# Kernel optimization log

Measured on AMD Instinct MI355X. Metric: run time of the kernel, lower is better.

The kernel has to match this reference:

```python
import jax, jax.numpy as jnp
import numpy as np

B, S, D = 16, 2048, 128


def setup_inputs() -> dict:
    key = jax.random.key(0)
    kq, kk, kv = jax.random.split(key, 3)
    return {
        "queries": jax.random.normal(kq, (B, S, D), dtype=jnp.float32),
        "keys": jax.random.normal(kk, (B, S, D), dtype=jnp.float32),
        "values": jax.random.normal(kv, (B, S, D), dtype=jnp.float32),
        "mask": jnp.zeros((B, S, S), dtype=bool),  # True -> masked out
    }


def reference(queries, keys, values, mask):
    d_k = queries.shape[-1]
    scale = 1.0 / np.sqrt(d_k).astype(np.float32)
    # scores: [B, S, S]
    scores = jnp.einsum("bqd,bkd->bqk", queries, keys) * scale
    scores = jnp.where(mask, -jnp.inf, scores)
    attn_weights = jax.nn.softmax(scores, axis=-1)
    # dropout prob = 0.0 (eval), identity
    output = jnp.einsum("bqk,bkd->bqd", attn_weights, values)
    return output
```

## Files before the change

### kernel.cpp

```cpp
#include <hip/hip_runtime.h>
#include <hip/hip_bf16.h>

#define SEQ    2048
#define DIM    128
#define NBATCH 16
#define KVB    64
#define HALFS  (SEQ / 2)
#define NTILE  (HALFS / KVB)
#define QW     16
#define NWAVE  8
#define QB     (QW * NWAVE)
#define NROW   (NBATCH * SEQ)
#define TELEM  (KVB * DIM)

typedef __bf16 bf16x8 __attribute__((ext_vector_type(8)));
typedef float  f32x4  __attribute__((ext_vector_type(4)));
typedef unsigned int uint;

#define LOG2E  1.44269504088896340736f
#define NEGINF (-__builtin_inff())

#define CVT_PK(d, lo, hi) asm("v_cvt_pk_bf16_f32 %0, %1, %2" : "=v"(d) : "v"(lo), "v"(hi))
#define SWAP32(x, y) asm("v_permlane32_swap_b32 %0, %1" : "+v"(x), "+v"(y))
#define SWAP16(x, y) asm("v_permlane16_swap_b32 %0, %1" : "+v"(x), "+v"(y))

typedef const __attribute__((address_space(1))) uint* gup;
typedef       __attribute__((address_space(3))) uint* lup;
#define GLDS16(g, l) __builtin_amdgcn_global_load_lds((gup)(g), (lup)(l), 16, 0, 0)

__global__ __launch_bounds__(512)
void sdpa_prep(const float* __restrict__ Kg, const float* __restrict__ Vg,
               __bf16* __restrict__ Kb, __bf16* __restrict__ Vb)
{
    const int tile = (int)blockIdx.x;
    const int tid  = (int)threadIdx.x;
    const size_t row0 = (size_t)tile * KVB;

    {
        const int kr = tid >> 3;
        const int c2 = (tid & 7) * 2;
        const int kx = kr & 7;
        const float* src = Kg + (row0 + kr) * DIM;
        __bf16* dst = Kb + ((size_t)tile * KVB + kr) * DIM;
        #pragma unroll
        for (int c = 0; c < 2; ++c) {
            const int ci = c2 + c;
            const int sc = ci ^ kx;
            const float4 a = *(const float4*)(src + sc * 8);
            const float4 b = *(const float4*)(src + sc * 8 + 4);
            bf16x8 h;
            h[0]=(__bf16)a.x; h[1]=(__bf16)a.y; h[2]=(__bf16)a.z; h[3]=(__bf16)a.w;
            h[4]=(__bf16)b.x; h[5]=(__bf16)b.y; h[6]=(__bf16)b.z; h[7]=(__bf16)b.w;
            *(bf16x8*)(dst + ci * 8) = h;
        }
    }
    {
        const int vd  = tid & 127;
        const int vks = tid >> 7;
        const int vx  = vd & 7;
        const float* src = Vg + row0 * DIM + vd;
        __bf16* dst = Vb + (size_t)tile * TELEM + (size_t)vd * KVB;
        #pragma unroll
        for (int c = 0; c < 2; ++c) {
            const int ck = vks * 2 + c;
            const int ci = ck ^ vx;
            bf16x8 h;
            #pragma unroll
            for (int j = 0; j < 8; ++j) h[j] = (__bf16)src[(size_t)(ck * 8 + j) * DIM];
            *(bf16x8*)(dst + ci * 8) = h;
        }
    }
}

__global__ __launch_bounds__(512, 4)
void sdpa_main(const float* __restrict__ Qg, const __bf16* __restrict__ Kbf,
               const __bf16* __restrict__ Vbf, const unsigned char* __restrict__ Mg,
               float* __restrict__ Uw, float* __restrict__ Lw)
{
    __shared__ __bf16 Ksh[2][TELEM];
    __shared__ __bf16 Vsh[2][TELEM];

    const int tid  = (int)threadIdx.x;
    const int wid  = tid >> 6;
    const int lane = tid & 63;
    const int lg   = lane >> 4;
    const int lr   = lane & 15;

    const int bid  = (int)blockIdx.x;
    const int nbid = (bid & 7) * 64 + (bid >> 3);
    const int half = nbid & 1;
    const int qt   = nbid >> 1;
    const int bb   = qt >> 4;
    const int q0w  = (qt & 15) * QB + wid * QW;

    const float qscale = 0.08838834764831845f * LOG2E;

    bf16x8 aq[4];
    {
        const float* qrow = Qg + ((size_t)(bb * SEQ + q0w + lr)) * DIM;
        #pragma unroll
        for (int kb = 0; kb < 4; ++kb) {
            const float4 f0 = *(const float4*)(qrow + kb * 32 + lg * 8);
            const float4 f1 = *(const float4*)(qrow + kb * 32 + lg * 8 + 4);
            bf16x8 h;
            h[0] = (__bf16)(f0.x * qscale); h[1] = (__bf16)(f0.y * qscale);
            h[2] = (__bf16)(f0.z * qscale); h[3] = (__bf16)(f0.w * qscale);
            h[4] = (__bf16)(f1.x * qscale); h[5] = (__bf16)(f1.y * qscale);
            h[6] = (__bf16)(f1.z * qscale); h[7] = (__bf16)(f1.w * qscale);
            aq[kb] = h;
        }
    }

    const __bf16* Kt0 = Kbf + (size_t)(bb * 32 + half * 16) * TELEM;
    const __bf16* Vt0 = Vbf + (size_t)(bb * 32 + half * 16) * TELEM;
    const unsigned char* Mrow = Mg + (size_t)bb * SEQ * SEQ
                              + (size_t)(q0w + lr) * SEQ + half * HALFS;

    uint mn0, mn1, mn2, mn3;

    const int woff0 = wid * 1024;
    const int woff1 = 8192 + wid * 1024;
    const int loff  = lane * 16;

    auto issue = [&](int t, int b) {
        const char* Ks = (const char*)(Kt0 + (size_t)t * TELEM);
        const char* Vs = (const char*)(Vt0 + (size_t)t * TELEM);
        char* Kd = (char*)Ksh[b];
        char* Vd = (char*)Vsh[b];
        GLDS16(Ks + woff0 + loff, Kd + woff0);
        GLDS16(Ks + woff1 + loff, Kd + woff1);
        GLDS16(Vs + woff0 + loff, Vd + woff0);
        GLDS16(Vs + woff1 + loff, Vd + woff1);
        const unsigned char* ms = Mrow + t * KVB + lg * 4;
        mn0 = *(const uint*)(ms);
        mn1 = *(const uint*)(ms + 16);
        mn2 = *(const uint*)(ms + 32);
        mn3 = *(const uint*)(ms + 48);
    };

    issue(0, 0);

    f32x4 acc[8];
    #pragma unroll
    for (int i = 0; i < 8; ++i) acc[i] = (f32x4)(0.0f);
    float l_run = 0.0f;

    const int kxr = lr & 7;

    for (int t = 0; t < NTILE; ++t) {
        asm volatile("s_waitcnt vmcnt(0)" ::: "memory");
        __syncthreads();
        const uint mw0 = mn0, mw1 = mn1, mw2 = mn2, mw3 = mn3;
        if (t + 1 < NTILE) issue(t + 1, (t + 1) & 1);

        const bf16x8* const Kc = (const bf16x8*)Ksh[t & 1];
        const bf16x8* const Vc = (const bf16x8*)Vsh[t & 1];

        f32x4 s0 = (f32x4)(0.0f), s1 = (f32x4)(0.0f);
        f32x4 s2 = (f32x4)(0.0f), s3 = (f32x4)(0.0f);
        __builtin_amdgcn_s_setprio(1);
        #pragma unroll
        for (int kb = 0; kb < 4; ++kb) {
            const int ch = (kb * 4 + lg) ^ kxr;
            const bf16x8 a0 = Kc[(lr)      * 16 + ch];
            const bf16x8 a1 = Kc[(16 + lr) * 16 + ch];
            const bf16x8 a2 = Kc[(32 + lr) * 16 + ch];
            const bf16x8 a3 = Kc[(48 + lr) * 16 + ch];
            s0 = __builtin_amdgcn_mfma_f32_16x16x32_bf16(a0, aq[kb], s0, 0, 0, 0);
            s1 = __builtin_amdgcn_mfma_f32_16x16x32_bf16(a1, aq[kb], s1, 0, 0, 0);
            s2 = __builtin_amdgcn_mfma_f32_16x16x32_bf16(a2, aq[kb], s2, 0, 0, 0);
            s3 = __builtin_amdgcn_mfma_f32_16x16x32_bf16(a3, aq[kb], s3, 0, 0, 0);
        }
        __builtin_amdgcn_s_setprio(0);

        if (mw0) {
            if (mw0 & 0x000000ffu) s0[0] = NEGINF;
            if (mw0 & 0x0000ff00u) s0[1] = NEGINF;
            if (mw0 & 0x00ff0000u) s0[2] = NEGINF;
            if (mw0 & 0xff000000u) s0[3] = NEGINF;
        }
        if (mw1) {
            if (mw1 & 0x000000ffu) s1[0] = NEGINF;
            if (mw1 & 0x0000ff00u) s1[1] = NEGINF;
            if (mw1 & 0x00ff0000u) s1[2] = NEGINF;
            if (mw1 & 0xff000000u) s1[3] = NEGINF;
        }
        if (mw2) {
            if (mw2 & 0x000000ffu) s2[0] = NEGINF;
            if (mw2 & 0x0000ff00u) s2[1] = NEGINF;
            if (mw2 & 0x00ff0000u) s2[2] = NEGINF;
            if (mw2 & 0xff000000u) s2[3] = NEGINF;
        }
        if (mw3) {
            if (mw3 & 0x000000ffu) s3[0] = NEGINF;
            if (mw3 & 0x0000ff00u) s3[1] = NEGINF;
            if (mw3 & 0x00ff0000u) s3[2] = NEGINF;
            if (mw3 & 0xff000000u) s3[3] = NEGINF;
        }

        float ps = 0.0f;
        #pragma unroll
        for (int r = 0; r < 4; ++r) { s0[r] = __builtin_amdgcn_exp2f(s0[r]); ps += s0[r]; }
        #pragma unroll
        for (int r = 0; r < 4; ++r) { s1[r] = __builtin_amdgcn_exp2f(s1[r]); ps += s1[r]; }
        #pragma unroll
        for (int r = 0; r < 4; ++r) { s2[r] = __builtin_amdgcn_exp2f(s2[r]); ps += s2[r]; }
        #pragma unroll
        for (int r = 0; r < 4; ++r) { s3[r] = __builtin_amdgcn_exp2f(s3[r]); ps += s3[r]; }
        l_run += ps;

        uint a0w, a1w, b0w, b1w, c0w, c1w, d0w, d1w;
        CVT_PK(a0w, s0[0], s0[1]); CVT_PK(a1w, s0[2], s0[3]);
        CVT_PK(b0w, s1[0], s1[1]); CVT_PK(b1w, s1[2], s1[3]);
        CVT_PK(c0w, s2[0], s2[1]); CVT_PK(c1w, s2[2], s2[3]);
        CVT_PK(d0w, s3[0], s3[1]); CVT_PK(d1w, s3[2], s3[3]);
        SWAP32(a0w, b0w); SWAP16(a0w, b0w);
        SWAP32(a1w, b1w); SWAP16(a1w, b1w);
        SWAP32(c0w, d0w); SWAP16(c0w, d0w);
        SWAP32(c1w, d1w); SWAP16(c1w, d1w);
        union W { uint w[4]; bf16x8 v; };
        W u0, u1;
        u0.w[0] = a0w; u0.w[1] = a1w; u0.w[2] = b0w; u0.w[3] = b1w;
        u1.w[0] = c0w; u1.w[1] = c1w; u1.w[2] = d0w; u1.w[3] = d1w;
        const bf16x8 ap0 = u0.v;
        const bf16x8 ap1 = u1.v;

        __builtin_amdgcn_s_setprio(1);
        #pragma unroll
        for (int nt = 0; nt < 8; ++nt) {
            const int rowb = (nt * 16 + lr) * 8;
            const bf16x8 bv0 = Vc[rowb + (lg ^ kxr)];
            acc[nt] = __builtin_amdgcn_mfma_f32_16x16x32_bf16(ap0, bv0, acc[nt], 0, 0, 0);
            const bf16x8 bv1 = Vc[rowb + ((4 + lg) ^ kxr)];
            acc[nt] = __builtin_amdgcn_mfma_f32_16x16x32_bf16(ap1, bv1, acc[nt], 0, 0, 0);
        }
        __builtin_amdgcn_s_setprio(0);
    }

    l_run += __shfl_xor(l_run, 16);
    l_run += __shfl_xor(l_run, 32);
    if (lg == 0)
        Lw[(size_t)half * NROW + bb * SEQ + q0w + lr] = l_run;

    float* ub = Uw + ((size_t)half * NROW + bb * SEQ + q0w + lg * 4) * DIM + lr;
    #pragma unroll
    for (int r = 0; r < 4; ++r)
        #pragma unroll
        for (int nt = 0; nt < 8; ++nt)
            ub[(size_t)r * DIM + nt * 16] = acc[nt][r];
}

__global__ __launch_bounds__(256)
void sdpa_combine(float* __restrict__ Og, const float* __restrict__ Uw,
                  const float* __restrict__ Lw)
{
    const int gid = (int)blockIdx.x * 256 + (int)threadIdx.x;
    const int row = gid >> 5;
    const float inv = 1.0f / (Lw[row] + Lw[NROW + row]);
    const float4* U0 = (const float4*)Uw;
    const float4* U1 = (const float4*)(Uw + (size_t)NROW * DIM);
    const float4 a = U0[gid];
    const float4 b = U1[gid];
    float4 o;
    o.x = (a.x + b.x) * inv; o.y = (a.y + b.y) * inv;
    o.z = (a.z + b.z) * inv; o.w = (a.w + b.w) * inv;
    ((float4*)Og)[gid] = o;
}

extern "C" void kernel_launch(void* const* d_in, const int* in_sizes, int n_in,
                              void* d_out, int out_size, void* d_ws, size_t ws_size,
                              hipStream_t stream) {
    const float* Q = (const float*)d_in[0];
    const float* K = (const float*)d_in[1];
    const float* V = (const float*)d_in[2];
    const unsigned char* M = (const unsigned char*)d_in[3];
    float* O  = (float*)d_out;
    float*  Uw  = (float*)d_ws;
    float*  Lw  = Uw + (size_t)2 * NROW * DIM;
    __bf16* Kbf = (__bf16*)(Lw + 2 * NROW);
    __bf16* Vbf = Kbf + (size_t)NROW * DIM;
    sdpa_prep<<<dim3(NROW / KVB), dim3(512), 0, stream>>>(K, V, Kbf, Vbf);
    sdpa_main<<<dim3(512), dim3(512), 0, stream>>>(Q, Kbf, Vbf, M, Uw, Lw);
    sdpa_combine<<<dim3(NROW * DIM / 4 / 256), dim3(256), 0, stream>>>(O, Uw, Lw);
}
```

Measured before the change: 75.21 us.

## Process two 16-row query groups per wave to reuse K/V LDS fragments

Each wave now handles 32 query rows as two 16-row groups instead of 16, and the block shrinks from 8 waves to 4 while keeping 128 query rows per block. Every K and V fragment read from LDS feeds two MFMAs, which halves LDS read traffic per unit of compute. The K/V tile copy is spread over fewer waves with more global-to-LDS loads each, and launch bounds move to 256 threads with fewer waves per SIMD. The cost is roughly double the accumulator and score registers, which lowers occupancy and the latency hiding that came from having more waves.

```diff
diff --git a/kernel.cpp b/kernel.cpp
--- a/kernel.cpp
+++ b/kernel.cpp
@@ -7,8 +7,8 @@
 #define KVB    64
 #define HALFS  (SEQ / 2)
 #define NTILE  (HALFS / KVB)
-#define QW     16
-#define NWAVE  8
+#define QW     32
+#define NWAVE  4
 #define QB     (QW * NWAVE)
 #define NROW   (NBATCH * SEQ)
 #define TELEM  (KVB * DIM)
@@ -27,6 +27,14 @@
 typedef const __attribute__((address_space(1))) uint* gup;
 typedef       __attribute__((address_space(3))) uint* lup;
 #define GLDS16(g, l) __builtin_amdgcn_global_load_lds((gup)(g), (lup)(l), 16, 0, 0)
+
+#define APPLY_MASK(mw, s)                          \
+    if (mw) {                                      \
+        if (mw & 0x000000ffu) s[0] = NEGINF;       \
+        if (mw & 0x0000ff00u) s[1] = NEGINF;       \
+        if (mw & 0x00ff0000u) s[2] = NEGINF;       \
+        if (mw & 0xff000000u) s[3] = NEGINF;       \
+    }
 
 __global__ __launch_bounds__(512)
 void sdpa_prep(const float* __restrict__ Kg, const float* __restrict__ Vg,
@@ -72,7 +80,7 @@
     }
 }
 
-__global__ __launch_bounds__(512, 4)
+__global__ __launch_bounds__(256, 2)
 void sdpa_main(const float* __restrict__ Qg, const __bf16* __restrict__ Kbf,
                const __bf16* __restrict__ Vbf, const unsigned char* __restrict__ Mg,
                float* __restrict__ Uw, float* __restrict__ Lw)
@@ -95,9 +103,10 @@
 
     const float qscale = 0.08838834764831845f * LOG2E;
 
-    bf16x8 aq[4];
-    {
-        const float* qrow = Qg + ((size_t)(bb * SEQ + q0w + lr)) * DIM;
+    bf16x8 aqA[4], aqB[4];
+    #pragma unroll
+    for (int g = 0; g < 2; ++g) {
+        const float* qrow = Qg + ((size_t)(bb * SEQ + q0w + g * 16 + lr)) * DIM;
         #pragma unroll
         for (int kb = 0; kb < 4; ++kb) {
             const float4 f0 = *(const float4*)(qrow + kb * 32 + lg * 8);
@@ -107,57 +116,65 @@
             h[2] = (__bf16)(f0.z * qscale); h[3] = (__bf16)(f0.w * qscale);
             h[4] = (__bf16)(f1.x * qscale); h[5] = (__bf16)(f1.y * qscale);
             h[6] = (__bf16)(f1.z * qscale); h[7] = (__bf16)(f1.w * qscale);
-            aq[kb] = h;
+            if (g == 0) aqA[kb] = h; else aqB[kb] = h;
         }
     }
 
     const __bf16* Kt0 = Kbf + (size_t)(bb * 32 + half * 16) * TELEM;
     const __bf16* Vt0 = Vbf + (size_t)(bb * 32 + half * 16) * TELEM;
-    const unsigned char* Mrow = Mg + (size_t)bb * SEQ * SEQ
-                              + (size_t)(q0w + lr) * SEQ + half * HALFS;
-
-    uint mn0, mn1, mn2, mn3;
-
-    const int woff0 = wid * 1024;
-    const int woff1 = 8192 + wid * 1024;
-    const int loff  = lane * 16;
+    const unsigned char* MrowA = Mg + (size_t)bb * SEQ * SEQ
+                               + (size_t)(q0w + lr) * SEQ + half * HALFS;
+    const unsigned char* MrowB = MrowA + (size_t)16 * SEQ;
+
+    uint mA0, mA1, mA2, mA3, mB0, mB1, mB2, mB3;
+    const int loff = lane * 16;
 
     auto issue = [&](int t, int b) {
         const char* Ks = (const char*)(Kt0 + (size_t)t * TELEM);
         const char* Vs = (const char*)(Vt0 + (size_t)t * TELEM);
         char* Kd = (char*)Ksh[b];
         char* Vd = (char*)Vsh[b];
-        GLDS16(Ks + woff0 + loff, Kd + woff0);
-        GLDS16(Ks + woff1 + loff, Kd + woff1);
-        GLDS16(Vs + woff0 + loff, Vd + woff0);
-        GLDS16(Vs + woff1 + loff, Vd + woff1);
-        const unsigned char* ms = Mrow + t * KVB + lg * 4;
-        mn0 = *(const uint*)(ms);
-        mn1 = *(const uint*)(ms + 16);
-        mn2 = *(const uint*)(ms + 32);
-        mn3 = *(const uint*)(ms + 48);
+        #pragma unroll
+        for (int j = 0; j < 4; ++j) {
+            const int o = wid * 1024 + j * 4096;
+            GLDS16(Ks + o + loff, Kd + o);
+            GLDS16(Vs + o + loff, Vd + o);
+        }
+        const unsigned char* msA = MrowA + t * KVB + lg * 4;
+        mA0 = *(const uint*)(msA);
+        mA1 = *(const uint*)(msA + 16);
+        mA2 = *(const uint*)(msA + 32);
+        mA3 = *(const uint*)(msA + 48);
+        const unsigned char* msB = MrowB + t * KVB + lg * 4;
+        mB0 = *(const uint*)(msB);
+        mB1 = *(const uint*)(msB + 16);
+        mB2 = *(const uint*)(msB + 32);
+        mB3 = *(const uint*)(msB + 48);
     };
 
     issue(0, 0);
 
-    f32x4 acc[8];
+    f32x4 accA[8], accB[8];
     #pragma unroll
-    for (int i = 0; i < 8; ++i) acc[i] = (f32x4)(0.0f);
-    float l_run = 0.0f;
+    for (int i = 0; i < 8; ++i) { accA[i] = (f32x4)(0.0f); accB[i] = (f32x4)(0.0f); }
+    float lA = 0.0f, lB = 0.0f;
 
     const int kxr = lr & 7;
 
     for (int t = 0; t < NTILE; ++t) {
         asm volatile("s_waitcnt vmcnt(0)" ::: "memory");
         __syncthreads();
-        const uint mw0 = mn0, mw1 = mn1, mw2 = mn2, mw3 = mn3;
+        const uint wA0 = mA0, wA1 = mA1, wA2 = mA2, wA3 = mA3;
+        const uint wB0 = mB0, wB1 = mB1, wB2 = mB2, wB3 = mB3;
         if (t + 1 < NTILE) issue(t + 1, (t + 1) & 1);
 
         const bf16x8* const Kc = (const bf16x8*)Ksh[t & 1];
         const bf16x8* const Vc = (const bf16x8*)Vsh[t & 1];
 
-        f32x4 s0 = (f32x4)(0.0f), s1 = (f32x4)(0.0f);
-        f32x4 s2 = (f32x4)(0.0f), s3 = (f32x4)(0.0f);
+        f32x4 sA0 = (f32x4)(0.0f), sA1 = (f32x4)(0.0f);
+        f32x4 sA2 = (f32x4)(0.0f), sA3 = (f32x4)(0.0f);
+        f32x4 sB0 = (f32x4)(0.0f), sB1 = (f32x4)(0.0f);
+        f32x4 sB2 = (f32x4)(0.0f), sB3 = (f32x4)(0.0f);
         __builtin_amdgcn_s_setprio(1);
         #pragma unroll
         for (int kb = 0; kb < 4; ++kb) {
@@ -166,88 +183,104 @@
             const bf16x8 a1 = Kc[(16 + lr) * 16 + ch];
             const bf16x8 a2 = Kc[(32 + lr) * 16 + ch];
             const bf16x8 a3 = Kc[(48 + lr) * 16 + ch];
-            s0 = __builtin_amdgcn_mfma_f32_16x16x32_bf16(a0, aq[kb], s0, 0, 0, 0);
-            s1 = __builtin_amdgcn_mfma_f32_16x16x32_bf16(a1, aq[kb], s1, 0, 0, 0);
-            s2 = __builtin_amdgcn_mfma_f32_16x16x32_bf16(a2, aq[kb], s2, 0, 0, 0);
-            s3 = __builtin_amdgcn_mfma_f32_16x16x32_bf16(a3, aq[kb], s3, 0, 0, 0);
+            sA0 = __builtin_amdgcn_mfma_f32_16x16x32_bf16(a0, aqA[kb], sA0, 0, 0, 0);
+            sB0 = __builtin_amdgcn_mfma_f32_16x16x32_bf16(a0, aqB[kb], sB0, 0, 0, 0);
+            sA1 = __builtin_amdgcn_mfma_f32_16x16x32_bf16(a1, aqA[kb], sA1, 0, 0, 0);
+            sB1 = __builtin_amdgcn_mfma_f32_16x16x32_bf16(a1, aqB[kb], sB1, 0, 0, 0);
+            sA2 = __builtin_amdgcn_mfma_f32_16x16x32_bf16(a2, aqA[kb], sA2, 0, 0, 0);
+            sB2 = __builtin_amdgcn_mfma_f32_16x16x32_bf16(a2, aqB[kb], sB2, 0, 0, 0);
+            sA3 = __builtin_amdgcn_mfma_f32_16x16x32_bf16(a3, aqA[kb], sA3, 0, 0, 0);
+            sB3 = __builtin_amdgcn_mfma_f32_16x16x32_bf16(a3, aqB[kb], sB3, 0, 0, 0);
         }
         __builtin_amdgcn_s_setprio(0);
 
-        if (mw0) {
-            if (mw0 & 0x000000ffu) s0[0] = NEGINF;
-            if (mw0 & 0x0000ff00u) s0[1] = NEGINF;
-            if (mw0 & 0x00ff0000u) s0[2] = NEGINF;
-            if (mw0 & 0xff000000u) s0[3] = NEGINF;
-        }
-        if (mw1) {
-            if (mw1 & 0x000000ffu) s1[0] = NEGINF;
-            if (mw1 & 0x0000ff00u) s1[1] = NEGINF;
-            if (mw1 & 0x00ff0000u) s1[2] = NEGINF;
-            if (mw1 & 0xff000000u) s1[3] = NEGINF;
-        }
-        if (mw2) {
-            if (mw2 & 0x000000ffu) s2[0] = NEGINF;
-            if (mw2 & 0x0000ff00u) s2[1] = NEGINF;
-            if (mw2 & 0x00ff0000u) s2[2] = NEGINF;
-            if (mw2 & 0xff000000u) s2[3] = NEGINF;
-        }
-        if (mw3) {
-            if (mw3 & 0x000000ffu) s3[0] = NEGINF;
-            if (mw3 & 0x0000ff00u) s3[1] = NEGINF;
-            if (mw3 & 0x00ff0000u) s3[2] = NEGINF;
-            if (mw3 & 0xff000000u) s3[3] = NEGINF;
-        }
-
-        float ps = 0.0f;
-        #pragma unroll
-        for (int r = 0; r < 4; ++r) { s0[r] = __builtin_amdgcn_exp2f(s0[r]); ps += s0[r]; }
-        #pragma unroll
-        for (int r = 0; r < 4; ++r) { s1[r] = __builtin_amdgcn_exp2f(s1[r]); ps += s1[r]; }
-        #pragma unroll
-        for (int r = 0; r < 4; ++r) { s2[r] = __builtin_amdgcn_exp2f(s2[r]); ps += s2[r]; }
-        #pragma unroll
-        for (int r = 0; r < 4; ++r) { s3[r] = __builtin_amdgcn_exp2f(s3[r]); ps += s3[r]; }
-        l_run += ps;
-
-        uint a0w, a1w, b0w, b1w, c0w, c1w, d0w, d1w;
-        CVT_PK(a0w, s0[0], s0[1]); CVT_PK(a1w, s0[2], s0[3]);
-        CVT_PK(b0w, s1[0], s1[1]); CVT_PK(b1w, s1[2], s1[3]);
-        CVT_PK(c0w, s2[0], s2[1]); CVT_PK(c1w, s2[2], s2[3]);
-        CVT_PK(d0w, s3[0], s3[1]); CVT_PK(d1w, s3[2], s3[3]);
-        SWAP32(a0w, b0w); SWAP16(a0w, b0w);
-        SWAP32(a1w, b1w); SWAP16(a1w, b1w);
-        SWAP32(c0w, d0w); SWAP16(c0w, d0w);
-        SWAP32(c1w, d1w); SWAP16(c1w, d1w);
-        union W { uint w[4]; bf16x8 v; };
-        W u0, u1;
-        u0.w[0] = a0w; u0.w[1] = a1w; u0.w[2] = b0w; u0.w[3] = b1w;
-        u1.w[0] = c0w; u1.w[1] = c1w; u1.w[2] = d0w; u1.w[3] = d1w;
-        const bf16x8 ap0 = u0.v;
-        const bf16x8 ap1 = u1.v;
+        APPLY_MASK(wA0, sA0) APPLY_MASK(wA1, sA1) APPLY_MASK(wA2, sA2) APPLY_MASK(wA3, sA3)
+        APPLY_MASK(wB0, sB0) APPLY_MASK(wB1, sB1) APPLY_MASK(wB2, sB2) APPLY_MASK(wB3, sB3)
+
+        float psA = 0.0f, psB = 0.0f;
+        #pragma unroll
+        for (int r = 0; r < 4; ++r) { sA0[r] = __builtin_amdgcn_exp2f(sA0[r]); psA += sA0[r]; }
+        #pragma unroll
+        for (int r = 0; r < 4; ++r) { sA1[r] = __builtin_amdgcn_exp2f(sA1[r]); psA += sA1[r]; }
+        #pragma unroll
+        for (int r = 0; r < 4; ++r) { sA2[r] = __builtin_amdgcn_exp2f(sA2[r]); psA += sA2[r]; }
+        #pragma unroll
+        for (int r = 0; r < 4; ++r) { sA3[r] = __builtin_amdgcn_exp2f(sA3[r]); psA += sA3[r]; }
+        #pragma unroll
+        for (int r = 0; r < 4; ++r) { sB0[r] = __builtin_amdgcn_exp2f(sB0[r]); psB += sB0[r]; }
+        #pragma unroll
+        for (int r = 0; r < 4; ++r) { sB1[r] = __builtin_amdgcn_exp2f(sB1[r]); psB += sB1[r]; }
+        #pragma unroll
+        for (int r = 0; r < 4; ++r) { sB2[r] = __builtin_amdgcn_exp2f(sB2[r]); psB += sB2[r]; }
+        #pragma unroll
+        for (int r = 0; r < 4; ++r) { sB3[r] = __builtin_amdgcn_exp2f(sB3[r]); psB += sB3[r]; }
+        lA += psA;
+        lB += psB;
+
+        bf16x8 apA0, apA1, apB0, apB1;
+        {
+            uint a0w, a1w, b0w, b1w, c0w, c1w, d0w, d1w;
+            CVT_PK(a0w, sA0[0], sA0[1]); CVT_PK(a1w, sA0[2], sA0[3]);
+            CVT_PK(b0w, sA1[0], sA1[1]); CVT_PK(b1w, sA1[2], sA1[3]);
+            CVT_PK(c0w, sA2[0], sA2[1]); CVT_PK(c1w, sA2[2], sA2[3]);
+            CVT_PK(d0w, sA3[0], sA3[1]); CVT_PK(d1w, sA3[2], sA3[3]);
+            SWAP32(a0w, b0w); SWAP16(a0w, b0w);
+            SWAP32(a1w, b1w); SWAP16(a1w, b1w);
+            SWAP32(c0w, d0w); SWAP16(c0w, d0w);
+            SWAP32(c1w, d1w); SWAP16(c1w, d1w);
+            union W { uint w[4]; bf16x8 v; };
+            W u0, u1;
+            u0.w[0] = a0w; u0.w[1] = a1w; u0.w[2] = b0w; u0.w[3] = b1w;
+            u1.w[0] = c0w; u1.w[1] = c1w; u1.w[2] = d0w; u1.w[3] = d1w;
+            apA0 = u0.v; apA1 = u1.v;
+        }
+        {
+            uint a0w, a1w, b0w, b1w, c0w, c1w, d0w, d1w;
+            CVT_PK(a0w, sB0[0], sB0[1]); CVT_PK(a1w, sB0[2], sB0[3]);
+            CVT_PK(b0w, sB1[0], sB1[1]); CVT_PK(b1w, sB1[2], sB1[3]);
+            CVT_PK(c0w, sB2[0], sB2[1]); CVT_PK(c1w, sB2[2], sB2[3]);
+            CVT_PK(d0w, sB3[0], sB3[1]); CVT_PK(d1w, sB3[2], sB3[3]);
+            SWAP32(a0w, b0w); SWAP16(a0w, b0w);
+            SWAP32(a1w, b1w); SWAP16(a1w, b1w);
+            SWAP32(c0w, d0w); SWAP16(c0w, d0w);
+            SWAP32(c1w, d1w); SWAP16(c1w, d1w);
+            union W { uint w[4]; bf16x8 v; };
+            W u0, u1;
+            u0.w[0] = a0w; u0.w[1] = a1w; u0.w[2] = b0w; u0.w[3] = b1w;
+            u1.w[0] = c0w; u1.w[1] = c1w; u1.w[2] = d0w; u1.w[3] = d1w;
+            apB0 = u0.v; apB1 = u1.v;
+        }
 
         __builtin_amdgcn_s_setprio(1);
         #pragma unroll
         for (int nt = 0; nt < 8; ++nt) {
             const int rowb = (nt * 16 + lr) * 8;
             const bf16x8 bv0 = Vc[rowb + (lg ^ kxr)];
-            acc[nt] = __builtin_amdgcn_mfma_f32_16x16x32_bf16(ap0, bv0, acc[nt], 0, 0, 0);
             const bf16x8 bv1 = Vc[rowb + ((4 + lg) ^ kxr)];
-            acc[nt] = __builtin_amdgcn_mfma_f32_16x16x32_bf16(ap1, bv1, acc[nt], 0, 0, 0);
+            accA[nt] = __builtin_amdgcn_mfma_f32_16x16x32_bf16(apA0, bv0, accA[nt], 0, 0, 0);
+            accA[nt] = __builtin_amdgcn_mfma_f32_16x16x32_bf16(apA1, bv1, accA[nt], 0, 0, 0);
+            accB[nt] = __builtin_amdgcn_mfma_f32_16x16x32_bf16(apB0, bv0, accB[nt], 0, 0, 0);
+            accB[nt] = __builtin_amdgcn_mfma_f32_16x16x32_bf16(apB1, bv1, accB[nt], 0, 0, 0);
         }
         __builtin_amdgcn_s_setprio(0);
     }
 
-    l_run += __shfl_xor(l_run, 16);
-    l_run += __shfl_xor(l_run, 32);
-    if (lg == 0)
-        Lw[(size_t)half * NROW + bb * SEQ + q0w + lr] = l_run;
-
-    float* ub = Uw + ((size_t)half * NROW + bb * SEQ + q0w + lg * 4) * DIM + lr;
+    lA += __shfl_xor(lA, 16); lA += __shfl_xor(lA, 32);
+    lB += __shfl_xor(lB, 16); lB += __shfl_xor(lB, 32);
+    if (lg == 0) {
+        Lw[(size_t)half * NROW + bb * SEQ + q0w + lr]      = lA;
+        Lw[(size_t)half * NROW + bb * SEQ + q0w + 16 + lr] = lB;
+    }
+
+    float* ubA = Uw + ((size_t)half * NROW + bb * SEQ + q0w + lg * 4) * DIM + lr;
+    float* ubB = ubA + (size_t)16 * DIM;
     #pragma unroll
     for (int r = 0; r < 4; ++r)
         #pragma unroll
-        for (int nt = 0; nt < 8; ++nt)
-            ub[(size_t)r * DIM + nt * 16] = acc[nt][r];
+        for (int nt = 0; nt < 8; ++nt) {
+            ubA[(size_t)r * DIM + nt * 16] = accA[nt][r];
+            ubB[(size_t)r * DIM + nt * 16] = accB[nt][r];
+        }
 }
 
 __global__ __launch_bounds__(256)
@@ -280,6 +313,6 @@
     __bf16* Kbf = (__bf16*)(Lw + 2 * NROW);
     __bf16* Vbf = Kbf + (size_t)NROW * DIM;
     sdpa_prep<<<dim3(NROW / KVB), dim3(512), 0, stream>>>(K, V, Kbf, Vbf);
-    sdpa_main<<<dim3(512), dim3(512), 0, stream>>>(Q, Kbf, Vbf, M, Uw, Lw);
+    sdpa_main<<<dim3(512), dim3(256), 0, stream>>>(Q, Kbf, Vbf, M, Uw, Lw);
     sdpa_combine<<<dim3(NROW * DIM / 4 / 256), dim3(256), 0, stream>>>(O, Uw, Lw);
 }
```

Result: no change. 76.44 us (+1.6%).

## Fuse split-KV combine into main kernel via last-arriver atomic counter

Applied to the files above, without the earlier changes.

Removes the separate combine kernel. Each of the two KV-half blocks for a query tile increments an atomic counter, and the second one to arrive reads the other half's partial output and row sum from workspace and writes the normalized output directly. This cuts one kernel launch and one full read/write pass over both partial buffers. In exchange it adds a thread fence, an atomic and extra syncs, and the counters are reset in the prep kernel.

```diff
diff --git a/kernel.cpp b/kernel.cpp
--- a/kernel.cpp
+++ b/kernel.cpp
@@ -12,6 +12,7 @@
 #define QB     (QW * NWAVE)
 #define NROW   (NBATCH * SEQ)
 #define TELEM  (KVB * DIM)
+#define NPAIR  (NROW / QB)
 
 typedef __bf16 bf16x8 __attribute__((ext_vector_type(8)));
 typedef float  f32x4  __attribute__((ext_vector_type(4)));
@@ -30,11 +31,14 @@
 
 __global__ __launch_bounds__(512)
 void sdpa_prep(const float* __restrict__ Kg, const float* __restrict__ Vg,
-               __bf16* __restrict__ Kb, __bf16* __restrict__ Vb)
+               __bf16* __restrict__ Kb, __bf16* __restrict__ Vb,
+               int* __restrict__ Fg)
 {
     const int tile = (int)blockIdx.x;
     const int tid  = (int)threadIdx.x;
     const size_t row0 = (size_t)tile * KVB;
+
+    if (tile == 0 && tid < NPAIR) Fg[tid] = 0;
 
     {
         const int kr = tid >> 3;
@@ -75,10 +79,12 @@
 __global__ __launch_bounds__(512, 4)
 void sdpa_main(const float* __restrict__ Qg, const __bf16* __restrict__ Kbf,
                const __bf16* __restrict__ Vbf, const unsigned char* __restrict__ Mg,
-               float* __restrict__ Uw, float* __restrict__ Lw)
+               float* __restrict__ Uw, float* __restrict__ Lw,
+               int* __restrict__ Fg, float* __restrict__ Og)
 {
     __shared__ __bf16 Ksh[2][TELEM];
     __shared__ __bf16 Vsh[2][TELEM];
+    __shared__ int s_old;
 
     const int tid  = (int)threadIdx.x;
     const int wid  = tid >> 6;
@@ -248,23 +254,31 @@
         #pragma unroll
         for (int nt = 0; nt < 8; ++nt)
             ub[(size_t)r * DIM + nt * 16] = acc[nt][r];
-}
-
-__global__ __launch_bounds__(256)
-void sdpa_combine(float* __restrict__ Og, const float* __restrict__ Uw,
-                  const float* __restrict__ Lw)
-{
-    const int gid = (int)blockIdx.x * 256 + (int)threadIdx.x;
-    const int row = gid >> 5;
-    const float inv = 1.0f / (Lw[row] + Lw[NROW + row]);
-    const float4* U0 = (const float4*)Uw;
-    const float4* U1 = (const float4*)(Uw + (size_t)NROW * DIM);
-    const float4 a = U0[gid];
-    const float4 b = U1[gid];
-    float4 o;
-    o.x = (a.x + b.x) * inv; o.y = (a.y + b.y) * inv;
-    o.z = (a.z + b.z) * inv; o.w = (a.w + b.w) * inv;
-    ((float4*)Og)[gid] = o;
+
+    __threadfence();
+    __syncthreads();
+    if (tid == 0) s_old = atomicAdd(&Fg[qt], 1);
+    __syncthreads();
+    if (s_old == 0) return;
+
+    __threadfence();
+
+    const int oh = half ^ 1;
+    const float* up = Uw + ((size_t)oh * NROW + bb * SEQ + q0w + lg * 4) * DIM + lr;
+    const float* lp = Lw + (size_t)oh * NROW + bb * SEQ + q0w;
+    float inv[4];
+    #pragma unroll
+    for (int r = 0; r < 4; ++r) {
+        const float lo = __shfl(l_run, (lane & 48) | (lg * 4 + r));
+        inv[r] = 1.0f / (lo + lp[lg * 4 + r]);
+    }
+    float* orow = Og + ((size_t)(bb * SEQ + q0w + lg * 4)) * DIM + lr;
+    #pragma unroll
+    for (int r = 0; r < 4; ++r)
+        #pragma unroll
+        for (int nt = 0; nt < 8; ++nt)
+            orow[(size_t)r * DIM + nt * 16] =
+                (acc[nt][r] + up[(size_t)r * DIM + nt * 16]) * inv[r];
 }
 
 extern "C" void kernel_launch(void* const* d_in, const int* in_sizes, int n_in,
@@ -277,9 +291,9 @@
     float* O  = (float*)d_out;
     float*  Uw  = (float*)d_ws;
     float*  Lw  = Uw + (size_t)2 * NROW * DIM;
-    __bf16* Kbf = (__bf16*)(Lw + 2 * NROW);
+    int*    Fg  = (int*)(Lw + (size_t)2 * NROW);
+    __bf16* Kbf = (__bf16*)(Fg + NPAIR);
     __bf16* Vbf = Kbf + (size_t)NROW * DIM;
-    sdpa_prep<<<dim3(NROW / KVB), dim3(512), 0, stream>>>(K, V, Kbf, Vbf);
-    sdpa_main<<<dim3(512), dim3(512), 0, stream>>>(Q, Kbf, Vbf, M, Uw, Lw);
-    sdpa_combine<<<dim3(NROW * DIM / 4 / 256), dim3(256), 0, stream>>>(O, Uw, Lw);
+    sdpa_prep<<<dim3(NROW / KVB), dim3(512), 0, stream>>>(K, V, Kbf, Vbf, Fg);
+    sdpa_main<<<dim3(512), dim3(512), 0, stream>>>(Q, Kbf, Vbf, M, Uw, Lw, Fg, O);
 }
```

Measured after the change: 254.8 us. +238.8%, slower.
